# Kernel tuning notes

Measured on AMD Instinct MI355X. Metric: run time of the kernel, lower is better.

## Reference

```python
import jax, jax.numpy as jnp
import numpy as np

N = 50000
E = 800000
F_IN = 128
H = 8        # heads
C = 32       # hidden_channels per head
HC = H * C   # 256
NEG_SLOPE = 0.2


def setup_inputs() -> dict:
    key = jax.random.key(0)
    ks = jax.random.split(key, 16)
    s = 0.1
    return {
        'x': jax.random.normal(ks[0], (N, F_IN), jnp.float32),
        'edge_index': jax.random.randint(ks[1], (2, E), 0, N, jnp.int64),
        'edge_weights': jax.random.uniform(ks[2], (E,), jnp.float32),
        'W1': jax.random.normal(ks[3], (F_IN, HC), jnp.float32) * s,
        'att_src1': jax.random.normal(ks[4], (H, C), jnp.float32) * s,
        'att_dst1': jax.random.normal(ks[5], (H, C), jnp.float32) * s,
        'b1': jnp.zeros((HC,), jnp.float32),
        'W2': jax.random.normal(ks[6], (HC, HC), jnp.float32) * s,
        'att_src2': jax.random.normal(ks[7], (H, C), jnp.float32) * s,
        'att_dst2': jax.random.normal(ks[8], (H, C), jnp.float32) * s,
        'b2': jnp.zeros((HC,), jnp.float32),
        'We': jax.random.normal(ks[9], (HC, 1), jnp.float32) * s,
        'be': jnp.zeros((1,), jnp.float32),
        'Wn': jax.random.normal(ks[10], (HC, 1), jnp.float32) * s,
        'bn': jnp.zeros((1,), jnp.float32),
    }


def gat_conv(x, src, dst, W, att_src, att_dst, bias):
    """PyG GATConv (concat=True, eval mode, self-loops already in src/dst)."""
    n = x.shape[0]
    h = (x @ W).reshape(n, H, C)                      # [N,H,C]
    a_s = jnp.sum(h * att_src, axis=-1)               # [N,H]
    a_d = jnp.sum(h * att_dst, axis=-1)               # [N,H]
    e = jax.nn.leaky_relu(a_s[src] + a_d[dst], NEG_SLOPE)  # [E',H]
    m = jax.ops.segment_max(e, dst, num_segments=n)   # segment softmax over dst
    ex = jnp.exp(e - m[dst])
    denom = jax.ops.segment_sum(ex, dst, num_segments=n)
    alpha = ex / (denom[dst] + 1e-16)                 # [E',H]
    out = jax.ops.segment_sum(alpha[..., None] * h[src], dst, num_segments=n)
    return out.reshape(n, HC) + bias


def reference(x, edge_index, edge_weights, W1, att_src1, att_dst1, b1,
              W2, att_src2, att_dst2, b2, We, be, Wn, bn):
    src0, dst0 = edge_index[0], edge_index[1]
    loops = jnp.arange(N, dtype=src0.dtype)
    src = jnp.concatenate([src0, loops])
    dst = jnp.concatenate([dst0, loops])
    # edge_weights is passed to GATConv as edge_attr but unused (edge_dim=None)
    h = jax.nn.relu(gat_conv(x, src, dst, W1, att_src1, att_dst1, b1))
    h = jax.nn.relu(gat_conv(h, src, dst, W2, att_src2, att_dst2, b2))
    edge_pred = (h[src0] * h[dst0]) @ We + be          # [E,1]
    node_pred = h @ Wn + bn                            # [N,1]
    return (edge_pred, node_pred)
```

## Files before the change

kernel.cpp:

```cpp
#include <hip/hip_runtime.h>
#include <hip/hip_bf16.h>

#define NN 50000
#define NE 800000
#define FIN 128
#define HC 256
#define NEG_SLOPE 0.2f

typedef short bf16x8 __attribute__((ext_vector_type(8)));
typedef float f32x4 __attribute__((ext_vector_type(4)));

__device__ __forceinline__ unsigned short f2bf(float f) {
  unsigned u = __float_as_uint(f);
  u += 0x7fff + ((u >> 16) & 1);
  return (unsigned short)(u >> 16);
}
__device__ __forceinline__ float bf2f(unsigned short s) {
  return __uint_as_float((unsigned)s << 16);
}
__device__ __forceinline__ float bflo(unsigned u) { return __uint_as_float(u << 16); }
__device__ __forceinline__ float bfhi(unsigned u) { return __uint_as_float(u & 0xffff0000u); }

__global__ __launch_bounds__(256) void convert_x(const float* __restrict__ X,
                                                 unsigned short* __restrict__ Xh,
                                                 unsigned short* __restrict__ Xl,
                                                 int n4) {
  int i = blockIdx.x * 256 + threadIdx.x;
  if (i >= n4) return;
  float4 v = ((const float4*)X)[i];
  ushort4 h, l;
  h.x = f2bf(v.x); l.x = f2bf(v.x - bf2f(h.x));
  h.y = f2bf(v.y); l.y = f2bf(v.y - bf2f(h.y));
  h.z = f2bf(v.z); l.z = f2bf(v.z - bf2f(h.z));
  h.w = f2bf(v.w); l.w = f2bf(v.w - bf2f(h.w));
  ((ushort4*)Xh)[i] = h;
  ((ushort4*)Xl)[i] = l;
}

__global__ __launch_bounds__(256) void convert_w(const float* __restrict__ W,
                                                 unsigned short* __restrict__ Wth,
                                                 unsigned short* __restrict__ Wtl,
                                                 int K) {
  int i = blockIdx.x * 256 + threadIdx.x;
  if (i >= K * HC) return;
  int k = i / HC, n = i % HC;
  float v = W[i];
  unsigned short h = f2bf(v);
  Wth[n * K + k] = h;
  Wtl[n * K + k] = f2bf(v - bf2f(h));
}

__global__ __launch_bounds__(256) void gemm_mfma(
    const unsigned short* __restrict__ Ah, const unsigned short* __restrict__ Al,
    const unsigned short* __restrict__ Bth, const unsigned short* __restrict__ Btl,
    unsigned short* __restrict__ Cb, int M, int K) {
  __shared__ unsigned short sAh[128 * 40];
  __shared__ unsigned short sAl[128 * 40];
  __shared__ unsigned short sBh[128 * 40];
  __shared__ unsigned short sBl[128 * 40];

  int t = threadIdx.x;
  int w = t >> 6, lane = t & 63;
  int quad = lane >> 4, lrow = lane & 15;
  int m0 = blockIdx.x * 128, n0 = blockIdx.y * 128;
  int wm = (w >> 1) * 64, wn = (w & 1) * 64;

  f32x4 acc[4][4] = {};

  for (int k0 = 0; k0 < K; k0 += 32) {
#pragma unroll
    for (int i = 0; i < 2; ++i) {
      int idx = t + i * 256;
      int row = idx >> 2, q = idx & 3;
      int gm = m0 + row;
      if (gm >= M) gm = M - 1;
      size_t ga = (size_t)gm * K + k0 + q * 8;
      size_t gb = (size_t)(n0 + row) * K + k0 + q * 8;
      *(uint4*)(sAh + row * 40 + q * 8) = *(const uint4*)(Ah + ga);
      *(uint4*)(sAl + row * 40 + q * 8) = *(const uint4*)(Al + ga);
      *(uint4*)(sBh + row * 40 + q * 8) = *(const uint4*)(Bth + gb);
      *(uint4*)(sBl + row * 40 + q * 8) = *(const uint4*)(Btl + gb);
    }
    __syncthreads();

    bf16x8 fah[4], fal[4];
#pragma unroll
    for (int mi = 0; mi < 4; ++mi) {
      fah[mi] = *(const bf16x8*)(sAh + (wm + mi * 16 + lrow) * 40 + quad * 8);
      fal[mi] = *(const bf16x8*)(sAl + (wm + mi * 16 + lrow) * 40 + quad * 8);
    }
#pragma unroll
    for (int ni = 0; ni < 4; ++ni) {
      bf16x8 fbh = *(const bf16x8*)(sBh + (wn + ni * 16 + lrow) * 40 + quad * 8);
      bf16x8 fbl = *(const bf16x8*)(sBl + (wn + ni * 16 + lrow) * 40 + quad * 8);
#pragma unroll
      for (int mi = 0; mi < 4; ++mi) {
        acc[mi][ni] = __builtin_amdgcn_mfma_f32_16x16x32_bf16(fah[mi], fbh, acc[mi][ni], 0, 0, 0);
        acc[mi][ni] = __builtin_amdgcn_mfma_f32_16x16x32_bf16(fah[mi], fbl, acc[mi][ni], 0, 0, 0);
        acc[mi][ni] = __builtin_amdgcn_mfma_f32_16x16x32_bf16(fal[mi], fbh, acc[mi][ni], 0, 0, 0);
      }
    }
    __syncthreads();
  }

#pragma unroll
  for (int mi = 0; mi < 4; ++mi) {
#pragma unroll
    for (int r = 0; r < 4; ++r) {
      int gm = m0 + wm + mi * 16 + quad * 4 + r;
      if (gm < M) {
#pragma unroll
        for (int ni = 0; ni < 4; ++ni) {
          int gn = n0 + wn + ni * 16 + lrow;
          Cb[(size_t)gm * HC + gn] = f2bf(acc[mi][ni][r]);
        }
      }
    }
  }
}

__global__ __launch_bounds__(256) void coef_kernel(
    const unsigned short* __restrict__ hb, const float* __restrict__ att_s,
    const float* __restrict__ att_d, float* __restrict__ a_s,
    float* __restrict__ a_d) {
  int n = blockIdx.x * 4 + (threadIdx.x >> 6);
  if (n >= NN) return;
  int lane = threadIdx.x & 63;
  uint2 q = ((const uint2*)(hb + (size_t)n * HC))[lane];
  float4 s4 = *(const float4*)(att_s + lane * 4);
  float4 d4 = *(const float4*)(att_d + lane * 4);
  float hx = bflo(q.x), hy = bfhi(q.x), hz = bflo(q.y), hw = bfhi(q.y);
  float ps = hx * s4.x + hy * s4.y + hz * s4.z + hw * s4.w;
  float pd = hx * d4.x + hy * d4.y + hz * d4.z + hw * d4.w;
#pragma unroll
  for (int off = 1; off <= 4; off <<= 1) {
    ps += __shfl_xor(ps, off);
    pd += __shfl_xor(pd, off);
  }
  if ((lane & 7) == 0) {
    a_s[n * 8 + (lane >> 3)] = ps;
    a_d[n * 8 + (lane >> 3)] = pd;
  }
}

__global__ void init_counts(int* counts, int* tmp) {
  int i = blockIdx.x * 256 + threadIdx.x;
  if (i < NN) { counts[i] = 1; tmp[i] = 0; }
}

__global__ void hist_kernel(const int* __restrict__ ei, int* __restrict__ counts) {
  int e = blockIdx.x * 256 + threadIdx.x;
  if (e < NE) atomicAdd(&counts[ei[NE + e]], 1);
}

__global__ void scan1(const int* __restrict__ counts, int* __restrict__ scanbuf,
                      int* __restrict__ bsum) {
  __shared__ int sd[256];
  int t = threadIdx.x;
  int i = blockIdx.x * 256 + t;
  int v = (i < NN) ? counts[i] : 0;
  sd[t] = v;
  __syncthreads();
#pragma unroll
  for (int off = 1; off < 256; off <<= 1) {
    int x = (t >= off) ? sd[t - off] : 0;
    __syncthreads();
    sd[t] += x;
    __syncthreads();
  }
  if (i < NN) scanbuf[i] = sd[t];
  if (t == 255) bsum[blockIdx.x] = sd[255];
}

__global__ void scan2(const int* __restrict__ bsum, int* __restrict__ boff, int nb) {
  __shared__ int sd[256];
  int t = threadIdx.x;
  int v = (t < nb) ? bsum[t] : 0;
  sd[t] = v;
  __syncthreads();
#pragma unroll
  for (int off = 1; off < 256; off <<= 1) {
    int x = (t >= off) ? sd[t - off] : 0;
    __syncthreads();
    sd[t] += x;
    __syncthreads();
  }
  if (t < nb) boff[t] = sd[t] - v;
}

__global__ void scan3(const int* __restrict__ scanbuf, const int* __restrict__ boff,
                      int* __restrict__ rowptr) {
  int i = blockIdx.x * 256 + threadIdx.x;
  if (i < NN) rowptr[i + 1] = scanbuf[i] + boff[blockIdx.x];
  if (i == 0) rowptr[0] = 0;
}

__global__ void scatter_kernel(const int* __restrict__ ei, const int* __restrict__ rowptr,
                               int* __restrict__ tmp, int* __restrict__ col,
                               int* __restrict__ eidv) {
  int e = blockIdx.x * 256 + threadIdx.x;
  if (e >= NE + NN) return;
  int s, d, id;
  if (e < NE) { s = ei[e]; d = ei[NE + e]; id = e; }
  else { s = d = e - NE; id = -1; }
  int pos = rowptr[d] + atomicAdd(&tmp[d], 1);
  col[pos] = s;
  eidv[pos] = id;
}

__global__ __launch_bounds__(256) void agg_kernel(
    const unsigned short* __restrict__ htb, const float* __restrict__ a_s,
    const float* __restrict__ a_d, const int* __restrict__ rowptr,
    const int* __restrict__ col, const float* __restrict__ bias,
    unsigned short* __restrict__ outb,
    unsigned short* __restrict__ outh, unsigned short* __restrict__ outl,
    const float* __restrict__ Wn, const float* __restrict__ bn,
    float* __restrict__ outn) {
  int d = blockIdx.x * 8 + (threadIdx.x >> 5);
  if (d >= NN) return;
  int l = threadIdx.x & 31;
  int hh = l >> 2;
  float adh = a_d[d * 8 + hh];
  int r0 = rowptr[d], r1 = rowptr[d + 1];
  float denom = 0.f;
  float4 acc0 = {0.f, 0.f, 0.f, 0.f};
  float4 acc1 = {0.f, 0.f, 0.f, 0.f};
  for (int r = r0; r < r1; r += 4) {
    int s[4];
    float as_[4];
    uint4 q[4];
    bool ok[4];
#pragma unroll
    for (int j = 0; j < 4; ++j) {
      int rj = r + j;
      ok[j] = rj < r1;
      rj = ok[j] ? rj : r1 - 1;
      s[j] = col[rj];
    }
#pragma unroll
    for (int j = 0; j < 4; ++j) {
      as_[j] = a_s[s[j] * 8 + hh];
      q[j] = ((const uint4*)(htb + (size_t)s[j] * HC))[l];
    }
#pragma unroll
    for (int j = 0; j < 4; ++j) {
      float e = as_[j] + adh;
      e = e > 0.f ? e : NEG_SLOPE * e;
      float w = ok[j] ? __expf(e) : 0.f;
      denom += w;
      acc0.x += w * bflo(q[j].x);
      acc0.y += w * bfhi(q[j].x);
      acc0.z += w * bflo(q[j].y);
      acc0.w += w * bfhi(q[j].y);
      acc1.x += w * bflo(q[j].z);
      acc1.y += w * bfhi(q[j].z);
      acc1.z += w * bflo(q[j].w);
      acc1.w += w * bfhi(q[j].w);
    }
  }
  float dv = 1.f / denom;
  float4 b0 = *(const float4*)(bias + l * 8);
  float4 b1 = *(const float4*)(bias + l * 8 + 4);
  float4 o0, o1;
  o0.x = fmaxf(fmaf(acc0.x, dv, b0.x), 0.f);
  o0.y = fmaxf(fmaf(acc0.y, dv, b0.y), 0.f);
  o0.z = fmaxf(fmaf(acc0.z, dv, b0.z), 0.f);
  o0.w = fmaxf(fmaf(acc0.w, dv, b0.w), 0.f);
  o1.x = fmaxf(fmaf(acc1.x, dv, b1.x), 0.f);
  o1.y = fmaxf(fmaf(acc1.y, dv, b1.y), 0.f);
  o1.z = fmaxf(fmaf(acc1.z, dv, b1.z), 0.f);
  o1.w = fmaxf(fmaf(acc1.w, dv, b1.w), 0.f);
  if (outb) {
    uint4 pb;
    pb.x = (unsigned)f2bf(o0.x) | ((unsigned)f2bf(o0.y) << 16);
    pb.y = (unsigned)f2bf(o0.z) | ((unsigned)f2bf(o0.w) << 16);
    pb.z = (unsigned)f2bf(o1.x) | ((unsigned)f2bf(o1.y) << 16);
    pb.w = (unsigned)f2bf(o1.z) | ((unsigned)f2bf(o1.w) << 16);
    ((uint4*)(outb + (size_t)d * HC))[l] = pb;
  }
  if (outh) {
    unsigned short h0 = f2bf(o0.x), h1 = f2bf(o0.y), h2 = f2bf(o0.z), h3 = f2bf(o0.w);
    unsigned short h4 = f2bf(o1.x), h5 = f2bf(o1.y), h6 = f2bf(o1.z), h7 = f2bf(o1.w);
    uint4 ph, pl;
    ph.x = (unsigned)h0 | ((unsigned)h1 << 16);
    ph.y = (unsigned)h2 | ((unsigned)h3 << 16);
    ph.z = (unsigned)h4 | ((unsigned)h5 << 16);
    ph.w = (unsigned)h6 | ((unsigned)h7 << 16);
    pl.x = (unsigned)f2bf(o0.x - bf2f(h0)) | ((unsigned)f2bf(o0.y - bf2f(h1)) << 16);
    pl.y = (unsigned)f2bf(o0.z - bf2f(h2)) | ((unsigned)f2bf(o0.w - bf2f(h3)) << 16);
    pl.z = (unsigned)f2bf(o1.x - bf2f(h4)) | ((unsigned)f2bf(o1.y - bf2f(h5)) << 16);
    pl.w = (unsigned)f2bf(o1.z - bf2f(h6)) | ((unsigned)f2bf(o1.w - bf2f(h7)) << 16);
    ((uint4*)(outh + (size_t)d * HC))[l] = ph;
    ((uint4*)(outl + (size_t)d * HC))[l] = pl;
  }
  if (outn) {
    const float4* wnp = (const float4*)(Wn + l * 8);
    float4 w0 = wnp[0], w1 = wnp[1];
    float p = o0.x * w0.x + o0.y * w0.y + o0.z * w0.z + o0.w * w0.w +
              o1.x * w1.x + o1.y * w1.y + o1.z * w1.z + o1.w * w1.w;
#pragma unroll
    for (int off = 1; off <= 16; off <<= 1) p += __shfl_xor(p, off);
    if (l == 0) outn[d] = p + bn[0];
  }
}

__global__ __launch_bounds__(256) void edge_pred_kernel(
    const unsigned short* __restrict__ h2b, const int* __restrict__ rowptr,
    const int* __restrict__ col, const int* __restrict__ eidv,
    const float* __restrict__ We, const float* __restrict__ be,
    float* __restrict__ out) {
  int d = blockIdx.x * 4 + (threadIdx.x >> 6);
  if (d >= NN) return;
  int lane = threadIdx.x & 63;
  int g = lane >> 4, l = lane & 15;
  float b = be[0];

  const uint4* rowd = (const uint4*)(h2b + (size_t)d * HC + l * 16);
  uint4 qd0 = rowd[0], qd1 = rowd[1];
  float wd[16];
  {
    const float4* wep = (const float4*)(We + l * 16);
    float4 w0 = wep[0], w1 = wep[1], w2 = wep[2], w3 = wep[3];
    wd[0] = bflo(qd0.x) * w0.x;  wd[1] = bfhi(qd0.x) * w0.y;
    wd[2] = bflo(qd0.y) * w0.z;  wd[3] = bfhi(qd0.y) * w0.w;
    wd[4] = bflo(qd0.z) * w1.x;  wd[5] = bfhi(qd0.z) * w1.y;
    wd[6] = bflo(qd0.w) * w1.z;  wd[7] = bfhi(qd0.w) * w1.w;
    wd[8] = bflo(qd1.x) * w2.x;  wd[9] = bfhi(qd1.x) * w2.y;
    wd[10] = bflo(qd1.y) * w2.z; wd[11] = bfhi(qd1.y) * w2.w;
    wd[12] = bflo(qd1.z) * w3.x; wd[13] = bfhi(qd1.z) * w3.y;
    wd[14] = bflo(qd1.w) * w3.z; wd[15] = bfhi(qd1.w) * w3.w;
  }

  int r0 = rowptr[d], r1 = rowptr[d + 1];
  for (int r = r0; r < r1; r += 8) {
    int rr0 = r + g, rr1 = r + 4 + g;
    int s0 = 0, id0 = -1, s1 = 0, id1 = -1;
    if (rr0 < r1) { s0 = col[rr0]; id0 = eidv[rr0]; }
    if (rr1 < r1) { s1 = col[rr1]; id1 = eidv[rr1]; }
    const uint4* ra = (const uint4*)(h2b + (size_t)s0 * HC + l * 16);
    const uint4* rb = (const uint4*)(h2b + (size_t)s1 * HC + l * 16);
    uint4 a0 = ra[0], a1 = ra[1];
    uint4 c0 = rb[0], c1 = rb[1];
    float p0 = bflo(a0.x) * wd[0] + bfhi(a0.x) * wd[1] + bflo(a0.y) * wd[2] +
               bfhi(a0.y) * wd[3] + bflo(a0.z) * wd[4] + bfhi(a0.z) * wd[5] +
               bflo(a0.w) * wd[6] + bfhi(a0.w) * wd[7] + bflo(a1.x) * wd[8] +
               bfhi(a1.x) * wd[9] + bflo(a1.y) * wd[10] + bfhi(a1.y) * wd[11] +
               bflo(a1.z) * wd[12] + bfhi(a1.z) * wd[13] + bflo(a1.w) * wd[14] +
               bfhi(a1.w) * wd[15];
    float p1 = bflo(c0.x) * wd[0] + bfhi(c0.x) * wd[1] + bflo(c0.y) * wd[2] +
               bfhi(c0.y) * wd[3] + bflo(c0.z) * wd[4] + bfhi(c0.z) * wd[5] +
               bflo(c0.w) * wd[6] + bfhi(c0.w) * wd[7] + bflo(c1.x) * wd[8] +
               bfhi(c1.x) * wd[9] + bflo(c1.y) * wd[10] + bfhi(c1.y) * wd[11] +
               bflo(c1.z) * wd[12] + bfhi(c1.z) * wd[13] + bflo(c1.w) * wd[14] +
               bfhi(c1.w) * wd[15];
#pragma unroll
    for (int off = 1; off <= 8; off <<= 1) {
      p0 += __shfl_xor(p0, off);
      p1 += __shfl_xor(p1, off);
    }
    if (l == 0) {
      if (id0 >= 0) out[id0] = p0 + b;
      if (id1 >= 0) out[id1] = p1 + b;
    }
  }
}

extern "C" void kernel_launch(void* const* d_in, const int* in_sizes, int n_in,
                              void* d_out, int out_size, void* d_ws, size_t ws_size,
                              hipStream_t stream) {
  const float* x  = (const float*)d_in[0];
  const int* ei   = (const int*)d_in[1];
  const float* W1 = (const float*)d_in[3];
  const float* as1 = (const float*)d_in[4];
  const float* ad1 = (const float*)d_in[5];
  const float* b1 = (const float*)d_in[6];
  const float* W2 = (const float*)d_in[7];
  const float* as2 = (const float*)d_in[8];
  const float* ad2 = (const float*)d_in[9];
  const float* b2 = (const float*)d_in[10];
  const float* We = (const float*)d_in[11];
  const float* be = (const float*)d_in[12];
  const float* Wn = (const float*)d_in[13];
  const float* bn = (const float*)d_in[14];
  float* out = (float*)d_out;

  char* wsp = (char*)d_ws;
  auto alloc = [&](size_t bytes) {
    char* p = wsp;
    wsp += (bytes + 255) & ~(size_t)255;
    return p;
  };
  unsigned short* hbA = (unsigned short*)alloc((size_t)NN * HC * 2);
  unsigned short* h1h = (unsigned short*)alloc((size_t)NN * HC * 2);
  unsigned short* h1l = (unsigned short*)alloc((size_t)NN * HC * 2);
  unsigned short* hbB = (unsigned short*)alloc((size_t)NN * HC * 2);
  float* a_s = (float*)alloc((size_t)NN * 8 * 4);
  float* a_d = (float*)alloc((size_t)NN * 8 * 4);
  int* rowptr = (int*)alloc((size_t)(NN + 1) * 4);
  int* colv = (int*)alloc((size_t)(NE + NN + 8) * 4);
  int* eidv = (int*)alloc((size_t)(NE + NN + 8) * 4);
  int* counts = (int*)alloc((size_t)NN * 4);
  int* tmp = (int*)alloc((size_t)NN * 4);
  int* scanbuf = (int*)alloc((size_t)NN * 4);
  int* bsum = (int*)alloc(256 * 4);
  int* boff = (int*)alloc(256 * 4);

  unsigned short* xh = h1h;
  unsigned short* xl = h1l;
  unsigned short* W1th = (unsigned short*)counts;
  unsigned short* W1tl = (unsigned short*)counts + FIN * HC;
  unsigned short* W2th = (unsigned short*)tmp;
  unsigned short* W2tl = (unsigned short*)scanbuf;

  const int NB = (NN + 255) / 256;

  init_counts<<<NB, 256, 0, stream>>>(counts, tmp);
  hist_kernel<<<(NE + 255) / 256, 256, 0, stream>>>(ei, counts);
  scan1<<<NB, 256, 0, stream>>>(counts, scanbuf, bsum);
  scan2<<<1, 256, 0, stream>>>(bsum, boff, NB);
  scan3<<<NB, 256, 0, stream>>>(scanbuf, boff, rowptr);
  scatter_kernel<<<(NE + NN + 255) / 256, 256, 0, stream>>>(ei, rowptr, tmp, colv, eidv);

  convert_x<<<(NN * FIN / 4 + 255) / 256, 256, 0, stream>>>(x, xh, xl, NN * FIN / 4);
  convert_w<<<(FIN * HC + 255) / 256, 256, 0, stream>>>(W1, W1th, W1tl, FIN);
  convert_w<<<(HC * HC + 255) / 256, 256, 0, stream>>>(W2, W2th, W2tl, HC);

  dim3 ggrid((NN + 127) / 128, 2);

  gemm_mfma<<<ggrid, 256, 0, stream>>>(xh, xl, W1th, W1tl, hbA, NN, FIN);
  coef_kernel<<<NN / 4, 256, 0, stream>>>(hbA, as1, ad1, a_s, a_d);
  agg_kernel<<<NN / 8, 256, 0, stream>>>(hbA, a_s, a_d, rowptr, colv, b1,
                                         (unsigned short*)nullptr, h1h, h1l,
                                         (const float*)nullptr, (const float*)nullptr,
                                         (float*)nullptr);

  gemm_mfma<<<ggrid, 256, 0, stream>>>(h1h, h1l, W2th, W2tl, hbA, NN, HC);
  coef_kernel<<<NN / 4, 256, 0, stream>>>(hbA, as2, ad2, a_s, a_d);
  agg_kernel<<<NN / 8, 256, 0, stream>>>(hbA, a_s, a_d, rowptr, colv, b2,
                                         hbB, (unsigned short*)nullptr,
                                         (unsigned short*)nullptr,
                                         Wn, bn, out + NE);

  edge_pred_kernel<<<NN / 4, 256, 0, stream>>>(hbB, rowptr, colv, eidv, We, be, out);
}
```

Baseline: 482.7 us.

## Fuse attention coefficients into GEMM epilogue and drop low-part activation splits

Folds the per-node attention dot products into the GEMM epilogue through shared-memory atomics, which removes the separate coef kernels and their re-read of the bf16 features. The activation operand A is now single bf16 rather than a hi/lo split, so each tile issues two MFMAs instead of three and no longer loads or stores the low-part arrays. The counts-init kernel is replaced with memsets, with the self-loop +1 moved into the scan. Precision drops because activation rounding error is no longer compensated, and the epilogue adds LDS atomic contention.

Measured after the change: 873.1 us. 1.81x slower.

```diff
diff --git a/kernel.cpp b/kernel.cpp
--- a/kernel.cpp
+++ b/kernel.cpp
@@ -23,18 +23,16 @@
 
 __global__ __launch_bounds__(256) void convert_x(const float* __restrict__ X,
                                                  unsigned short* __restrict__ Xh,
-                                                 unsigned short* __restrict__ Xl,
                                                  int n4) {
   int i = blockIdx.x * 256 + threadIdx.x;
   if (i >= n4) return;
   float4 v = ((const float4*)X)[i];
-  ushort4 h, l;
-  h.x = f2bf(v.x); l.x = f2bf(v.x - bf2f(h.x));
-  h.y = f2bf(v.y); l.y = f2bf(v.y - bf2f(h.y));
-  h.z = f2bf(v.z); l.z = f2bf(v.z - bf2f(h.z));
-  h.w = f2bf(v.w); l.w = f2bf(v.w - bf2f(h.w));
+  ushort4 h;
+  h.x = f2bf(v.x);
+  h.y = f2bf(v.y);
+  h.z = f2bf(v.z);
+  h.w = f2bf(v.w);
   ((ushort4*)Xh)[i] = h;
-  ((ushort4*)Xl)[i] = l;
 }
 
 __global__ __launch_bounds__(256) void convert_w(const float* __restrict__ W,
@@ -50,20 +48,27 @@
   Wtl[n * K + k] = f2bf(v - bf2f(h));
 }
 
-__global__ __launch_bounds__(256) void gemm_mfma(
-    const unsigned short* __restrict__ Ah, const unsigned short* __restrict__ Al,
-    const unsigned short* __restrict__ Bth, const unsigned short* __restrict__ Btl,
-    unsigned short* __restrict__ Cb, int M, int K) {
-  __shared__ unsigned short sAh[128 * 40];
-  __shared__ unsigned short sAl[128 * 40];
+__global__ __launch_bounds__(256) void gemm_coef(
+    const unsigned short* __restrict__ A, const unsigned short* __restrict__ Bth,
+    const unsigned short* __restrict__ Btl, const float* __restrict__ att_s,
+    const float* __restrict__ att_d, unsigned short* __restrict__ Cb,
+    float* __restrict__ a_s, float* __restrict__ a_d, int M, int K) {
+  __shared__ unsigned short sA[128 * 40];
   __shared__ unsigned short sBh[128 * 40];
   __shared__ unsigned short sBl[128 * 40];
+  __shared__ float sAS[128][4];
+  __shared__ float sAD[128][4];
 
   int t = threadIdx.x;
   int w = t >> 6, lane = t & 63;
   int quad = lane >> 4, lrow = lane & 15;
   int m0 = blockIdx.x * 128, n0 = blockIdx.y * 128;
   int wm = (w >> 1) * 64, wn = (w & 1) * 64;
+
+  if (t < 128) {
+#pragma unroll
+    for (int j = 0; j < 4; ++j) { sAS[t][j] = 0.f; sAD[t][j] = 0.f; }
+  }
 
   f32x4 acc[4][4] = {};
 
@@ -76,28 +81,24 @@
       if (gm >= M) gm = M - 1;
       size_t ga = (size_t)gm * K + k0 + q * 8;
       size_t gb = (size_t)(n0 + row) * K + k0 + q * 8;
-      *(uint4*)(sAh + row * 40 + q * 8) = *(const uint4*)(Ah + ga);
-      *(uint4*)(sAl + row * 40 + q * 8) = *(const uint4*)(Al + ga);
+      *(uint4*)(sA + row * 40 + q * 8) = *(const uint4*)(A + ga);
       *(uint4*)(sBh + row * 40 + q * 8) = *(const uint4*)(Bth + gb);
       *(uint4*)(sBl + row * 40 + q * 8) = *(const uint4*)(Btl + gb);
     }
     __syncthreads();
 
-    bf16x8 fah[4], fal[4];
-#pragma unroll
-    for (int mi = 0; mi < 4; ++mi) {
-      fah[mi] = *(const bf16x8*)(sAh + (wm + mi * 16 + lrow) * 40 + quad * 8);
-      fal[mi] = *(const bf16x8*)(sAl + (wm + mi * 16 + lrow) * 40 + quad * 8);
-    }
+    bf16x8 fa[4];
+#pragma unroll
+    for (int mi = 0; mi < 4; ++mi)
+      fa[mi] = *(const bf16x8*)(sA + (wm + mi * 16 + lrow) * 40 + quad * 8);
 #pragma unroll
     for (int ni = 0; ni < 4; ++ni) {
       bf16x8 fbh = *(const bf16x8*)(sBh + (wn + ni * 16 + lrow) * 40 + quad * 8);
       bf16x8 fbl = *(const bf16x8*)(sBl + (wn + ni * 16 + lrow) * 40 + quad * 8);
 #pragma unroll
       for (int mi = 0; mi < 4; ++mi) {
-        acc[mi][ni] = __builtin_amdgcn_mfma_f32_16x16x32_bf16(fah[mi], fbh, acc[mi][ni], 0, 0, 0);
-        acc[mi][ni] = __builtin_amdgcn_mfma_f32_16x16x32_bf16(fah[mi], fbl, acc[mi][ni], 0, 0, 0);
-        acc[mi][ni] = __builtin_amdgcn_mfma_f32_16x16x32_bf16(fal[mi], fbh, acc[mi][ni], 0, 0, 0);
+        acc[mi][ni] = __builtin_amdgcn_mfma_f32_16x16x32_bf16(fa[mi], fbh, acc[mi][ni], 0, 0, 0);
+        acc[mi][ni] = __builtin_amdgcn_mfma_f32_16x16x32_bf16(fa[mi], fbl, acc[mi][ni], 0, 0, 0);
       }
     }
     __syncthreads();
@@ -107,45 +108,34 @@
   for (int mi = 0; mi < 4; ++mi) {
 #pragma unroll
     for (int r = 0; r < 4; ++r) {
-      int gm = m0 + wm + mi * 16 + quad * 4 + r;
+      int lr = wm + mi * 16 + quad * 4 + r;
+      int gm = m0 + lr;
       if (gm < M) {
 #pragma unroll
         for (int ni = 0; ni < 4; ++ni) {
-          int gn = n0 + wn + ni * 16 + lrow;
-          Cb[(size_t)gm * HC + gn] = f2bf(acc[mi][ni][r]);
+          int lc = wn + ni * 16 + lrow;
+          int gn = n0 + lc;
+          float v = acc[mi][ni][r];
+          Cb[(size_t)gm * HC + gn] = f2bf(v);
+          int hd = lc >> 5;
+          atomicAdd(&sAS[lr][hd], v * att_s[gn]);
+          atomicAdd(&sAD[lr][hd], v * att_d[gn]);
         }
       }
     }
   }
-}
-
-__global__ __launch_bounds__(256) void coef_kernel(
-    const unsigned short* __restrict__ hb, const float* __restrict__ att_s,
-    const float* __restrict__ att_d, float* __restrict__ a_s,
-    float* __restrict__ a_d) {
-  int n = blockIdx.x * 4 + (threadIdx.x >> 6);
-  if (n >= NN) return;
-  int lane = threadIdx.x & 63;
-  uint2 q = ((const uint2*)(hb + (size_t)n * HC))[lane];
-  float4 s4 = *(const float4*)(att_s + lane * 4);
-  float4 d4 = *(const float4*)(att_d + lane * 4);
-  float hx = bflo(q.x), hy = bfhi(q.x), hz = bflo(q.y), hw = bfhi(q.y);
-  float ps = hx * s4.x + hy * s4.y + hz * s4.z + hw * s4.w;
-  float pd = hx * d4.x + hy * d4.y + hz * d4.z + hw * d4.w;
-#pragma unroll
-  for (int off = 1; off <= 4; off <<= 1) {
-    ps += __shfl_xor(ps, off);
-    pd += __shfl_xor(pd, off);
-  }
-  if ((lane & 7) == 0) {
-    a_s[n * 8 + (lane >> 3)] = ps;
-    a_d[n * 8 + (lane >> 3)] = pd;
-  }
-}
-
-__global__ void init_counts(int* counts, int* tmp) {
-  int i = blockIdx.x * 256 + threadIdx.x;
-  if (i < NN) { counts[i] = 1; tmp[i] = 0; }
+  __syncthreads();
+  if (t < 128) {
+    int gm = m0 + t;
+    if (gm < M) {
+      int hb = n0 >> 5;
+#pragma unroll
+      for (int j = 0; j < 4; ++j) {
+        a_s[gm * 8 + hb + j] = sAS[t][j];
+        a_d[gm * 8 + hb + j] = sAD[t][j];
+      }
+    }
+  }
 }
 
 __global__ void hist_kernel(const int* __restrict__ ei, int* __restrict__ counts) {
@@ -158,7 +148,7 @@
   __shared__ int sd[256];
   int t = threadIdx.x;
   int i = blockIdx.x * 256 + t;
-  int v = (i < NN) ? counts[i] : 0;
+  int v = (i < NN) ? counts[i] + 1 : 0;
   sd[t] = v;
   __syncthreads();
 #pragma unroll
@@ -213,7 +203,6 @@
     const float* __restrict__ a_d, const int* __restrict__ rowptr,
     const int* __restrict__ col, const float* __restrict__ bias,
     unsigned short* __restrict__ outb,
-    unsigned short* __restrict__ outh, unsigned short* __restrict__ outl,
     const float* __restrict__ Wn, const float* __restrict__ bn,
     float* __restrict__ outn) {
   int d = blockIdx.x * 8 + (threadIdx.x >> 5);
@@ -270,29 +259,12 @@
   o1.y = fmaxf(fmaf(acc1.y, dv, b1.y), 0.f);
   o1.z = fmaxf(fmaf(acc1.z, dv, b1.z), 0.f);
   o1.w = fmaxf(fmaf(acc1.w, dv, b1.w), 0.f);
-  if (outb) {
-    uint4 pb;
-    pb.x = (unsigned)f2bf(o0.x) | ((unsigned)f2bf(o0.y) << 16);
-    pb.y = (unsigned)f2bf(o0.z) | ((unsigned)f2bf(o0.w) << 16);
-    pb.z = (unsigned)f2bf(o1.x) | ((unsigned)f2bf(o1.y) << 16);
-    pb.w = (unsigned)f2bf(o1.z) | ((unsigned)f2bf(o1.w) << 16);
-    ((uint4*)(outb + (size_t)d * HC))[l] = pb;
-  }
-  if (outh) {
-    unsigned short h0 = f2bf(o0.x), h1 = f2bf(o0.y), h2 = f2bf(o0.z), h3 = f2bf(o0.w);
-    unsigned short h4 = f2bf(o1.x), h5 = f2bf(o1.y), h6 = f2bf(o1.z), h7 = f2bf(o1.w);
-    uint4 ph, pl;
-    ph.x = (unsigned)h0 | ((unsigned)h1 << 16);
-    ph.y = (unsigned)h2 | ((unsigned)h3 << 16);
-    ph.z = (unsigned)h4 | ((unsigned)h5 << 16);
-    ph.w = (unsigned)h6 | ((unsigned)h7 << 16);
-    pl.x = (unsigned)f2bf(o0.x - bf2f(h0)) | ((unsigned)f2bf(o0.y - bf2f(h1)) << 16);
-    pl.y = (unsigned)f2bf(o0.z - bf2f(h2)) | ((unsigned)f2bf(o0.w - bf2f(h3)) << 16);
-    pl.z = (unsigned)f2bf(o1.x - bf2f(h4)) | ((unsigned)f2bf(o1.y - bf2f(h5)) << 16);
-    pl.w = (unsigned)f2bf(o1.z - bf2f(h6)) | ((unsigned)f2bf(o1.w - bf2f(h7)) << 16);
-    ((uint4*)(outh + (size_t)d * HC))[l] = ph;
-    ((uint4*)(outl + (size_t)d * HC))[l] = pl;
-  }
+  uint4 pb;
+  pb.x = (unsigned)f2bf(o0.x) | ((unsigned)f2bf(o0.y) << 16);
+  pb.y = (unsigned)f2bf(o0.z) | ((unsigned)f2bf(o0.w) << 16);
+  pb.z = (unsigned)f2bf(o1.x) | ((unsigned)f2bf(o1.y) << 16);
+  pb.w = (unsigned)f2bf(o1.z) | ((unsigned)f2bf(o1.w) << 16);
+  ((uint4*)(outb + (size_t)d * HC))[l] = pb;
   if (outn) {
     const float4* wnp = (const float4*)(Wn + l * 8);
     float4 w0 = wnp[0], w1 = wnp[1];
@@ -391,8 +363,7 @@
     return p;
   };
   unsigned short* hbA = (unsigned short*)alloc((size_t)NN * HC * 2);
-  unsigned short* h1h = (unsigned short*)alloc((size_t)NN * HC * 2);
-  unsigned short* h1l = (unsigned short*)alloc((size_t)NN * HC * 2);
+  unsigned short* h1b = (unsigned short*)alloc((size_t)NN * HC * 2);
   unsigned short* hbB = (unsigned short*)alloc((size_t)NN * HC * 2);
   float* a_s = (float*)alloc((size_t)NN * 8 * 4);
   float* a_d = (float*)alloc((size_t)NN * 8 * 4);
@@ -405,8 +376,7 @@
   int* bsum = (int*)alloc(256 * 4);
   int* boff = (int*)alloc(256 * 4);
 
-  unsigned short* xh = h1h;
-  unsigned short* xl = h1l;
+  unsigned short* xh = h1b;
   unsigned short* W1th = (unsigned short*)counts;
   unsigned short* W1tl = (unsigned short*)counts + FIN * HC;
   unsigned short* W2th = (unsigned short*)tmp;
@@ -414,31 +384,27 @@
 
   const int NB = (NN + 255) / 256;
 
-  init_counts<<<NB, 256, 0, stream>>>(counts, tmp);
+  hipMemsetAsync(counts, 0, (size_t)NN * 4, stream);
+  hipMemsetAsync(tmp, 0, (size_t)NN * 4, stream);
   hist_kernel<<<(NE + 255) / 256, 256, 0, stream>>>(ei, counts);
   scan1<<<NB, 256, 0, stream>>>(counts, scanbuf, bsum);
   scan2<<<1, 256, 0, stream>>>(bsum, boff, NB);
   scan3<<<NB, 256, 0, stream>>>(scanbuf, boff, rowptr);
   scatter_kernel<<<(NE + NN + 255) / 256, 256, 0, stream>>>(ei, rowptr, tmp, colv, eidv);
 
-  convert_x<<<(NN * FIN / 4 + 255) / 256, 256, 0, stream>>>(x, xh, xl, NN * FIN / 4);
+  convert_x<<<(NN * FIN / 4 + 255) / 256, 256, 0, stream>>>(x, xh, NN * FIN / 4);
   convert_w<<<(FIN * HC + 255) / 256, 256, 0, stream>>>(W1, W1th, W1tl, FIN);
   convert_w<<<(HC * HC + 255) / 256, 256, 0, stream>>>(W2, W2th, W2tl, HC);
 
   dim3 ggrid((NN + 127) / 128, 2);
 
-  gemm_mfma<<<ggrid, 256, 0, stream>>>(xh, xl, W1th, W1tl, hbA, NN, FIN);
-  coef_kernel<<<NN / 4, 256, 0, stream>>>(hbA, as1, ad1, a_s, a_d);
-  agg_kernel<<<NN / 8, 256, 0, stream>>>(hbA, a_s, a_d, rowptr, colv, b1,
-                                         (unsigned short*)nullptr, h1h, h1l,
+  gemm_coef<<<ggrid, 256, 0, stream>>>(xh, W1th, W1tl, as1, ad1, hbA, a_s, a_d, NN, FIN);
+  agg_kernel<<<NN / 8, 256, 0, stream>>>(hbA, a_s, a_d, rowptr, colv, b1, h1b,
                                          (const float*)nullptr, (const float*)nullptr,
                                          (float*)nullptr);
 
-  gemm_mfma<<<ggrid, 256, 0, stream>>>(h1h, h1l, W2th, W2tl, hbA, NN, HC);
-  coef_kernel<<<NN / 4, 256, 0, stream>>>(hbA, as2, ad2, a_s, a_d);
-  agg_kernel<<<NN / 8, 256, 0, stream>>>(hbA, a_s, a_d, rowptr, colv, b2,
-                                         hbB, (unsigned short*)nullptr,
-                                         (unsigned short*)nullptr,
+  gemm_coef<<<ggrid, 256, 0, stream>>>(h1b, W2th, W2tl, as2, ad2, hbA, a_s, a_d, NN, HC);
+  agg_kernel<<<NN / 8, 256, 0, stream>>>(hbA, a_s, a_d, rowptr, colv, b2, hbB,
                                          Wn, bn, out + NE);
 
   edge_pred_kernel<<<NN / 4, 256, 0, stream>>>(hbB, rowptr, colv, eidv, We, be, out);
```
